# Performance work log

Measured on AMD Instinct MI355X. Metric: run time of the kernel, lower is better.

The kernel has to match this reference:

```python
import jax, jax.numpy as jnp
import numpy as np

B, S, d, D = 128, 1024, 64, 64  # batch, seq_len, physical dim, bond dim


def setup_inputs() -> dict:
    key = jax.random.key(0)
    k1, k2, k3, k4 = jax.random.split(key, 4)
    k_core = (d * D * D) ** (-0.5)
    k_vec = d ** (-0.5)
    core = k_core * jax.random.normal(k1, (d, D, D), dtype=jnp.float32)
    left_boundary = k_vec * jax.random.normal(k2, (D,), dtype=jnp.float32)
    right_boundary = k_vec * jax.random.normal(k3, (D,), dtype=jnp.float32)
    X = jax.random.randint(k4, (B, S), 0, d, dtype=jnp.int32)
    return {"X": X, "core": core, "left_boundary": left_boundary,
            "right_boundary": right_boundary}


def reference(X, core, left_boundary, right_boundary):
    """Faithful JAX version of TTrain._log_contract_at_batch (homogeneous).

    X: [B, S] int category indices; core: [d, D, D]; boundaries: [D].
    Returns logprobs: [B].
    The per-step normalization (infinity-norm) + accumulated log-norm trick of
    the original is preserved exactly; the final
    log((exp(lognorm) * out)**2) is computed in the mathematically identical
    stable form 2*(lognorm + log|out|).
    """
    batch = X.shape[0]
    lb = jnp.broadcast_to(left_boundary, (batch, left_boundary.shape[0]))  # [B, D]
    Z0 = jnp.max(jnp.abs(lb), axis=1)                                      # [B]
    c0 = lb / Z0[:, None]
    logn0 = jnp.log(Z0)

    def step(carry, x_t):
        c, logn = carry                       # c: [B, D]
        w_t = core[x_t]                       # gather selected cores: [B, D, D]
        ct = jnp.einsum('bi,bij->bj', c, w_t)  # [B, D]
        Zt = jnp.max(jnp.abs(ct), axis=1)      # [B] infinity norm
        return (ct / Zt[:, None], logn + jnp.log(Zt)), None

    (c, logn), _ = jax.lax.scan(step, (c0, logn0), X.T)  # scan over seq axis
    out = jnp.einsum('bi,i->b', c, right_boundary)        # [B]
    logprobs = 2.0 * (logn + jnp.log(jnp.abs(out)))
    return logprobs
```

## Files before the change

### kernel.cpp

```cpp
#include <hip/hip_runtime.h>
#include <math.h>


#define TT_S 1024
#define TT_D 64
#define NCHUNK 32
#define CLEN 32

typedef __attribute__((ext_vector_type(8))) short short8;
typedef __attribute__((ext_vector_type(4))) float float4v;
typedef __attribute__((ext_vector_type(4))) unsigned uint4v;
typedef __attribute__((ext_vector_type(2))) unsigned uint2v;

static __device__ __forceinline__ short8 as_short8(uint4v u) {
    union { uint4v u; short8 s; } x; x.u = u; return x.s;
}

__global__ __launch_bounds__(64) void tt_prep(
    const float* __restrict__ core, short* __restrict__ tblA,
    short* __restrict__ tblBt)
{
    const int x = blockIdx.x, l = threadIdx.x;
    const int n = l & 15, q = l >> 4;
    const float* W = core + x * 4096;

    #pragma unroll
    for (int I = 0; I < 4; ++I)
        #pragma unroll
        for (int Kp = 0; Kp < 2; ++Kp) {
            short8 v;
            const int row = 16 * I + n;
            const int c0 = 32 * Kp + 4 * q;
            #pragma unroll
            for (int j = 0; j < 8; ++j) {
                const int col = c0 + 16 * (j >> 2) + (j & 3);
                v[j] = (short)(__float_as_uint(W[row * 64 + col]) >> 16);
            }
            *(short8*)(tblA + ((size_t)(x * 8 + I * 2 + Kp) * 64 + l) * 8) = v;
        }
    #pragma unroll
    for (int Kp = 0; Kp < 2; ++Kp)
        #pragma unroll
        for (int J = 0; J < 4; ++J) {
            short8 v;
            const int col = 16 * J + n;
            const int r0 = 32 * Kp + 4 * q;
            #pragma unroll
            for (int j = 0; j < 8; ++j) {
                const int row = r0 + 16 * (j >> 2) + (j & 3);
                v[j] = (short)(__float_as_uint(W[row * 64 + col]) >> 16);
            }
            *(short8*)(tblBt + ((size_t)(x * 8 + Kp * 4 + J) * 64 + l) * 8) = v;
        }
}

__global__ __launch_bounds__(64, 4) void tt_stage1(
    const int* __restrict__ X, const short* __restrict__ tblA,
    const short* __restrict__ tblBt, short* __restrict__ PT,
    float* __restrict__ ln1)
{
    const int w = blockIdx.x;
    const int b = w / NCHUNK, chunk = w % NCHUNK;
    const int l = threadIdx.x, n = l & 15, q = l >> 4;
    const int* Xc = X + b * TT_S + chunk * CLEN;

    const float4v zero = {0.f, 0.f, 0.f, 0.f};
    float4v acc[4][4];
    short8 Bf[8], Af[8];
    float logn = 0.f;

    #define LOAD_FRAGS(DST, TBL, XIDX)                                        \
    {   const short8* p_ = (const short8*)((TBL) + (size_t)(XIDX) * 4096) + l; \
        _Pragma("unroll")                                                     \
        for (int f_ = 0; f_ < 8; ++f_) (DST)[f_] = p_[f_ * 64]; }

    #define MFMA_ALL(ABUF)                                                    \
        _Pragma("unroll")                                                     \
        for (int I_ = 0; I_ < 4; ++I_)                                        \
            _Pragma("unroll")                                                 \
            for (int J_ = 0; J_ < 4; ++J_) {                                  \
                float4v c0_ = __builtin_amdgcn_mfma_f32_16x16x32_bf16(        \
                    (ABUF)[2 * I_ + 0], Bf[J_], zero, 0, 0, 0);               \
                acc[I_][J_] = __builtin_amdgcn_mfma_f32_16x16x32_bf16(        \
                    (ABUF)[2 * I_ + 1], Bf[4 + J_], c0_, 0, 0, 0);            \
            }

    #define PACK_BF()                                                         \
        _Pragma("unroll")                                                     \
        for (int Kp_ = 0; Kp_ < 2; ++Kp_)                                     \
            _Pragma("unroll")                                                 \
            for (int J_ = 0; J_ < 4; ++J_) {                                  \
                uint4v u_;                                                    \
                u_[0] = __builtin_amdgcn_perm(                                \
                    __float_as_uint(acc[2 * Kp_][J_][1]),                     \
                    __float_as_uint(acc[2 * Kp_][J_][0]), 0x07060302u);       \
                u_[1] = __builtin_amdgcn_perm(                                \
                    __float_as_uint(acc[2 * Kp_][J_][3]),                     \
                    __float_as_uint(acc[2 * Kp_][J_][2]), 0x07060302u);       \
                u_[2] = __builtin_amdgcn_perm(                                \
                    __float_as_uint(acc[2 * Kp_ + 1][J_][1]),                 \
                    __float_as_uint(acc[2 * Kp_ + 1][J_][0]), 0x07060302u);   \
                u_[3] = __builtin_amdgcn_perm(                                \
                    __float_as_uint(acc[2 * Kp_ + 1][J_][3]),                 \
                    __float_as_uint(acc[2 * Kp_ + 1][J_][2]), 0x07060302u);   \
                Bf[Kp_ * 4 + J_] = as_short8(u_);                             \
            }

    #define RENORM()                                                          \
    {   float Z_ = 0.f;                                                       \
        _Pragma("unroll")                                                     \
        for (int I_ = 0; I_ < 4; ++I_)                                        \
            _Pragma("unroll")                                                 \
            for (int J_ = 0; J_ < 4; ++J_)                                    \
                _Pragma("unroll")                                             \
                for (int r_ = 0; r_ < 4; ++r_)                                \
                    Z_ = fmaxf(Z_, fabsf(acc[I_][J_][r_]));                   \
        _Pragma("unroll")                                                     \
        for (int m_ = 32; m_; m_ >>= 1) Z_ = fmaxf(Z_, __shfl_xor(Z_, m_));   \
        logn += logf(Z_);                                                     \
        const float rZ_ = 1.0f / Z_;                                          \
        _Pragma("unroll")                                                     \
        for (int I_ = 0; I_ < 4; ++I_)                                        \
            _Pragma("unroll")                                                 \
            for (int J_ = 0; J_ < 4; ++J_)                                    \
                _Pragma("unroll")                                             \
                for (int r_ = 0; r_ < 4; ++r_) acc[I_][J_][r_] *= rZ_; }

    LOAD_FRAGS(Bf, tblBt, Xc[CLEN - 1])
    LOAD_FRAGS(Af, tblA, Xc[CLEN - 2])
    MFMA_ALL(Af)

    #pragma unroll 1
    for (int s = 1; s < CLEN - 1; ++s) {
        LOAD_FRAGS(Af, tblA, Xc[CLEN - 2 - s])
        asm volatile("" ::: "memory");
        if ((s & 7) == 0) RENORM()
        PACK_BF()
        MFMA_ALL(Af)
    }

    {
        float Z = 0.f;
        #pragma unroll
        for (int I = 0; I < 4; ++I)
            #pragma unroll
            for (int J = 0; J < 4; ++J)
                #pragma unroll
                for (int r = 0; r < 4; ++r) Z = fmaxf(Z, fabsf(acc[I][J][r]));
        #pragma unroll
        for (int m = 32; m; m >>= 1) Z = fmaxf(Z, __shfl_xor(Z, m));
        logn += logf(Z);
        const float rZ = 1.0f / Z;
        short* base = PT + (size_t)w * 4096;
        #pragma unroll
        for (int I = 0; I < 4; ++I)
            #pragma unroll
            for (int J = 0; J < 4; ++J) {
                float4v v = acc[I][J];
                #pragma unroll
                for (int r = 0; r < 4; ++r) v[r] *= rZ;
                uint2v dd;
                dd[0] = __builtin_amdgcn_perm(__float_as_uint(v[1]),
                                              __float_as_uint(v[0]), 0x07060302u);
                dd[1] = __builtin_amdgcn_perm(__float_as_uint(v[3]),
                                              __float_as_uint(v[2]), 0x07060302u);
                *(uint2v*)(base + (16 * J + n) * 64 + 16 * I + 4 * q) = dd;
            }
        if (l == 0) ln1[w] = logn;
    }
    #undef LOAD_FRAGS
    #undef MFMA_ALL
    #undef PACK_BF
    #undef RENORM
}

__global__ __launch_bounds__(64, 1) void tt_stage2(
    const short* __restrict__ PT, const float* __restrict__ ln1,
    const float* __restrict__ lb, const float* __restrict__ rb,
    float* __restrict__ out)
{
    __shared__ float cb[64];
    const int b = blockIdx.x, j = threadIdx.x;

    float c = lb[j];
    float Z = fabsf(c);
    #pragma unroll
    for (int m = 32; m; m >>= 1) Z = fmaxf(Z, __shfl_xor(Z, m));
    float logn = logf(Z);
    c *= (1.0f / Z);

    float ln = (j < NCHUNK) ? ln1[b * NCHUNK + j] : 0.f;
    #pragma unroll
    for (int m = 32; m; m >>= 1) ln += __shfl_xor(ln, m);
    logn += ln;

    const short* base = PT + (size_t)b * NCHUNK * 4096 + j * 64;

    short8 bufA[8], bufB[8];
    #pragma unroll
    for (int f = 0; f < 8; ++f) bufA[f] = ((const short8*)base)[f];

    #define S2_STEP(BUF)                                                      \
    {                                                                         \
        cb[j] = c;                                                            \
        asm volatile("s_waitcnt lgkmcnt(0)" ::: "memory");                    \
        float a0 = 0.f, a1 = 0.f, a2 = 0.f, a3 = 0.f;                         \
        _Pragma("unroll")                                                     \
        for (int f = 0; f < 8; ++f) {                                         \
            union { short8 s; uint4v u; } uu; uu.s = (BUF)[f];                \
            const float4v cv0 = *(const float4v*)(cb + 8 * f);                \
            const float4v cv1 = *(const float4v*)(cb + 8 * f + 4);            \
            a0 = fmaf(cv0[0], __uint_as_float(uu.u[0] << 16), a0);            \
            a1 = fmaf(cv0[1], __uint_as_float(uu.u[0] & 0xffff0000u), a1);    \
            a2 = fmaf(cv0[2], __uint_as_float(uu.u[1] << 16), a2);            \
            a3 = fmaf(cv0[3], __uint_as_float(uu.u[1] & 0xffff0000u), a3);    \
            a0 = fmaf(cv1[0], __uint_as_float(uu.u[2] << 16), a0);            \
            a1 = fmaf(cv1[1], __uint_as_float(uu.u[2] & 0xffff0000u), a1);    \
            a2 = fmaf(cv1[2], __uint_as_float(uu.u[3] << 16), a2);            \
            a3 = fmaf(cv1[3], __uint_as_float(uu.u[3] & 0xffff0000u), a3);    \
        }                                                                     \
        float cn = (a0 + a1) + (a2 + a3);                                     \
        float Zl = fabsf(cn);                                                 \
        _Pragma("unroll")                                                     \
        for (int m = 32; m; m >>= 1) Zl = fmaxf(Zl, __shfl_xor(Zl, m));       \
        logn += logf(Zl);                                                     \
        c = cn * (1.0f / Zl);                                                 \
    }

    #pragma unroll 1
    for (int k = 0; k < NCHUNK; k += 2) {
        {   const short8* p = (const short8*)(base + (size_t)(k + 1) * 4096);
            #pragma unroll
            for (int f = 0; f < 8; ++f) bufB[f] = p[f];
        }
        asm volatile("" ::: "memory");
        S2_STEP(bufA)
        {   const int kn = (k + 2 < NCHUNK) ? (k + 2) : (NCHUNK - 1);
            const short8* p = (const short8*)(base + (size_t)kn * 4096);
            #pragma unroll
            for (int f = 0; f < 8; ++f) bufA[f] = p[f];
        }
        asm volatile("" ::: "memory");
        S2_STEP(bufB)
    }
    #undef S2_STEP

    float dot = c * rb[j];
    #pragma unroll
    for (int m = 32; m; m >>= 1) dot += __shfl_xor(dot, m);
    if (j == 0) out[b] = 2.0f * (logn + logf(fabsf(dot)));
}

__global__ __launch_bounds__(256) void tt_transpose(
    const float* __restrict__ core, float* __restrict__ coreT)
{
    __shared__ float tile[64][65];
    const int x = blockIdx.x;
    const float* src = core + x * 4096;
    float* dst = coreT + x * 4096;
    const int r0 = threadIdx.x >> 6, cc = threadIdx.x & 63;
    #pragma unroll
    for (int k = 0; k < 16; ++k) tile[r0 + 4 * k][cc] = src[(r0 + 4 * k) * 64 + cc];
    __syncthreads();
    #pragma unroll
    for (int k = 0; k < 16; ++k) dst[(r0 + 4 * k) * 64 + cc] = tile[cc][r0 + 4 * k];
}

__global__ __launch_bounds__(64, 1) void ttrain_chain2(
    const int* __restrict__ X, const float* __restrict__ coreT,
    const float* __restrict__ lb, const float* __restrict__ rb,
    float* __restrict__ out)
{
    __shared__ float cbuf[2][64];
    const int b = blockIdx.x, j = threadIdx.x;
    const int* Xrow = X + b * TT_S;
    float c = lb[j];
    float Z = fabsf(c);
    #pragma unroll
    for (int m = 32; m; m >>= 1) Z = fmaxf(Z, __shfl_xor(Z, m));
    float logn = logf(Z);
    c *= (1.0f / Z);
    const float* colbase = coreT + j * 64;
    int xs_cur = Xrow[j];
    int xs_nxt = Xrow[64 + j];
    float4 wA[16], wB[16];
    {
        const int x0 = Xrow[0];
        const float4* p = (const float4*)(colbase + x0 * 4096);
        #pragma unroll
        for (int k = 0; k < 16; ++k) wA[k] = p[k];
    }
    #define TT_STEP(WCUR, WNXT, SLOT, XNEXT, T)                              \
    {                                                                        \
        cbuf[SLOT][j] = c;                                                   \
        {                                                                    \
            const float4* pre = (const float4*)(colbase + (XNEXT) * 4096);   \
            _Pragma("unroll")                                                \
            for (int k = 0; k < 16; ++k) WNXT[k] = pre[k];                   \
        }                                                                    \
        asm volatile("s_waitcnt lgkmcnt(0)" ::: "memory");                   \
        float a0 = 0.f, a1 = 0.f, a2 = 0.f, a3 = 0.f;                        \
        const float4* cb2 = (const float4*)cbuf[SLOT];                       \
        _Pragma("unroll")                                                    \
        for (int k = 0; k < 16; ++k) {                                       \
            float4 cv = cb2[k];                                              \
            a0 = fmaf(cv.x, WCUR[k].x, a0);                                  \
            a1 = fmaf(cv.y, WCUR[k].y, a1);                                  \
            a2 = fmaf(cv.z, WCUR[k].z, a2);                                  \
            a3 = fmaf(cv.w, WCUR[k].w, a3);                                  \
        }                                                                    \
        float cn = (a0 + a1) + (a2 + a3);                                    \
        if (((T) & 7) == 7) {                                                \
            float Zl = fabsf(cn);                                            \
            _Pragma("unroll")                                                \
            for (int m = 32; m; m >>= 1) Zl = fmaxf(Zl, __shfl_xor(Zl, m));  \
            logn += logf(Zl);                                                \
            cn *= (1.0f / Zl);                                               \
        }                                                                    \
        c = cn;                                                              \
    }
    for (int tc = 0; tc < TT_S; tc += 64) {
        #pragma unroll 1
        for (int u = 0; u < 64; u += 2) {
            const int x1 = __builtin_amdgcn_readlane(xs_cur, u + 1);
            TT_STEP(wA, wB, 0, x1, tc + u)
            const int src2 = (u + 2 < 64) ? xs_cur : xs_nxt;
            const int x2 = __builtin_amdgcn_readlane(src2, (u + 2) & 63);
            TT_STEP(wB, wA, 1, x2, tc + u + 1)
        }
        xs_cur = xs_nxt;
        const int nc = tc + 128;
        xs_nxt = Xrow[((nc < TT_S) ? nc : 0) + j];
    }
    #undef TT_STEP
    float dot = c * rb[j];
    #pragma unroll
    for (int m = 32; m; m >>= 1) dot += __shfl_xor(dot, m);
    if (j == 0) out[b] = 2.0f * (logn + logf(fabsf(dot)));
}

extern "C" void kernel_launch(void* const* d_in, const int* in_sizes, int n_in,
                              void* d_out, int out_size, void* d_ws, size_t ws_size,
                              hipStream_t stream) {
    const int*   X    = (const int*)d_in[0];
    const float* core = (const float*)d_in[1];
    const float* lb   = (const float*)d_in[2];
    const float* rb   = (const float*)d_in[3];
    float* out = (float*)d_out;

    const int B = in_sizes[0] / TT_S;
    const size_t tblBytes = (size_t)64 * 8 * 64 * 8 * sizeof(short);
    const size_t ptBytes  = (size_t)B * NCHUNK * 4096 * sizeof(short);
    const size_t lnBytes  = (size_t)B * NCHUNK * sizeof(float);
    const size_t need = 2 * tblBytes + ptBytes + lnBytes;

    if (ws_size >= need) {
        char* w = (char*)d_ws;
        short* tblA  = (short*)w;
        short* tblBt = (short*)(w + tblBytes);
        short* PT    = (short*)(w + 2 * tblBytes);
        float* ln1   = (float*)(w + 2 * tblBytes + ptBytes);
        tt_prep<<<64, 64, 0, stream>>>(core, tblA, tblBt);
        tt_stage1<<<B * NCHUNK, 64, 0, stream>>>(X, tblA, tblBt, PT, ln1);
        tt_stage2<<<B, 64, 0, stream>>>(PT, ln1, lb, rb, out);
    } else if (ws_size >= (size_t)64 * 4096 * sizeof(float)) {
        float* coreT = (float*)d_ws;
        tt_transpose<<<64, 256, 0, stream>>>(core, coreT);
        ttrain_chain2<<<B, TT_D, 0, stream>>>(X, coreT, lb, rb, out);
    }
}
```

Before: 154.0 us.

## Fuse stage2 into stage1 via last-block atomic counter and double-buffer A fragments

Removes the separate stage2 launch. Each stage1 block increments a per-batch atomic counter, and the last chunk block of each batch runs the sequential combine of the chunk matrices. The stage1 inner loop also double-buffers the A fragments, so the next step's loads are issued before the current MFMAs and load latency overlaps with compute. The cost is more registers (launch bounds lowered from 4 to 3 waves), counter zeroing in the prep kernel, and a serial tail on the last block per batch.

After: 449.9 us. +192.1%, slower.

```diff
diff --git a/kernel.cpp b/kernel.cpp
--- a/kernel.cpp
+++ b/kernel.cpp
@@ -18,12 +18,17 @@
 
 __global__ __launch_bounds__(64) void tt_prep(
     const float* __restrict__ core, short* __restrict__ tblA,
-    short* __restrict__ tblBt)
+    short* __restrict__ tblBt, int* __restrict__ ctr)
 {
     const int x = blockIdx.x, l = threadIdx.x;
     const int n = l & 15, q = l >> 4;
     const float* W = core + x * 4096;
 
+    if (x == 0) {
+        #pragma unroll
+        for (int k = 0; k < 4; ++k) ctr[l + 64 * k] = 0;
+    }
+
     #pragma unroll
     for (int I = 0; I < 4; ++I)
         #pragma unroll
@@ -54,11 +59,14 @@
         }
 }
 
-__global__ __launch_bounds__(64, 4) void tt_stage1(
+__global__ __launch_bounds__(64, 3) void tt_stage1(
     const int* __restrict__ X, const short* __restrict__ tblA,
     const short* __restrict__ tblBt, short* __restrict__ PT,
-    float* __restrict__ ln1)
+    float* __restrict__ ln1, int* __restrict__ ctr,
+    const float* __restrict__ lb, const float* __restrict__ rb,
+    float* __restrict__ out)
 {
+    __shared__ float cb[64];
     const int w = blockIdx.x;
     const int b = w / NCHUNK, chunk = w % NCHUNK;
     const int l = threadIdx.x, n = l & 15, q = l >> 4;
@@ -66,7 +74,7 @@
 
     const float4v zero = {0.f, 0.f, 0.f, 0.f};
     float4v acc[4][4];
-    short8 Bf[8], Af[8];
+    short8 Bf[8], A0[8], A1[8];
     float logn = 0.f;
 
     #define LOAD_FRAGS(DST, TBL, XIDX)                                        \
@@ -127,16 +135,27 @@
                 for (int r_ = 0; r_ < 4; ++r_) acc[I_][J_][r_] *= rZ_; }
 
     LOAD_FRAGS(Bf, tblBt, Xc[CLEN - 1])
-    LOAD_FRAGS(Af, tblA, Xc[CLEN - 2])
-    MFMA_ALL(Af)
+    LOAD_FRAGS(A0, tblA, Xc[CLEN - 2])
+    LOAD_FRAGS(A1, tblA, Xc[CLEN - 3])
+
+    MFMA_ALL(A0)
+    LOAD_FRAGS(A0, tblA, Xc[CLEN - 4])
 
     #pragma unroll 1
-    for (int s = 1; s < CLEN - 1; ++s) {
-        LOAD_FRAGS(Af, tblA, Xc[CLEN - 2 - s])
-        asm volatile("" ::: "memory");
-        if ((s & 7) == 0) RENORM()
+    for (int it = 0; it < (CLEN - 2) / 2; ++it) {
         PACK_BF()
-        MFMA_ALL(Af)
+        MFMA_ALL(A1)
+        {
+            const int tn = CLEN - 6 - 2 * it;
+            LOAD_FRAGS(A1, tblA, Xc[tn < 0 ? 0 : tn])
+        }
+        if (((2 * it + 2) & 7) == 0) RENORM()
+        PACK_BF()
+        MFMA_ALL(A0)
+        {
+            const int tn = CLEN - 7 - 2 * it;
+            LOAD_FRAGS(A0, tblA, Xc[tn < 0 ? 0 : tn])
+        }
     }
 
     {
@@ -172,37 +191,36 @@
     #undef MFMA_ALL
     #undef PACK_BF
     #undef RENORM
-}
-
-__global__ __launch_bounds__(64, 1) void tt_stage2(
-    const short* __restrict__ PT, const float* __restrict__ ln1,
-    const float* __restrict__ lb, const float* __restrict__ rb,
-    float* __restrict__ out)
-{
-    __shared__ float cb[64];
-    const int b = blockIdx.x, j = threadIdx.x;
-
-    float c = lb[j];
+
+    __threadfence();
+    int last = 0;
+    if (l == 0) last = (atomicAdd(&ctr[b], 1) == NCHUNK - 1) ? 1 : 0;
+    last = __shfl(last, 0);
+    if (!last) return;
+    __threadfence();
+
+    float c = lb[l];
     float Z = fabsf(c);
     #pragma unroll
     for (int m = 32; m; m >>= 1) Z = fmaxf(Z, __shfl_xor(Z, m));
-    float logn = logf(Z);
+    float lg = logf(Z);
     c *= (1.0f / Z);
 
-    float ln = (j < NCHUNK) ? ln1[b * NCHUNK + j] : 0.f;
-    #pragma unroll
-    for (int m = 32; m; m >>= 1) ln += __shfl_xor(ln, m);
-    logn += ln;
-
-    const short* base = PT + (size_t)b * NCHUNK * 4096 + j * 64;
-
+    {
+        float ln = (l < NCHUNK) ? ln1[b * NCHUNK + l] : 0.f;
+        #pragma unroll
+        for (int m = 32; m; m >>= 1) ln += __shfl_xor(ln, m);
+        lg += ln;
+    }
+
+    const short* base2 = PT + (size_t)b * NCHUNK * 4096 + l * 64;
     short8 bufA[8], bufB[8];
     #pragma unroll
-    for (int f = 0; f < 8; ++f) bufA[f] = ((const short8*)base)[f];
+    for (int f = 0; f < 8; ++f) bufA[f] = ((const short8*)base2)[f];
 
     #define S2_STEP(BUF)                                                      \
     {                                                                         \
-        cb[j] = c;                                                            \
+        cb[l] = c;                                                            \
         asm volatile("s_waitcnt lgkmcnt(0)" ::: "memory");                    \
         float a0 = 0.f, a1 = 0.f, a2 = 0.f, a3 = 0.f;                         \
         _Pragma("unroll")                                                     \
@@ -223,20 +241,20 @@
         float Zl = fabsf(cn);                                                 \
         _Pragma("unroll")                                                     \
         for (int m = 32; m; m >>= 1) Zl = fmaxf(Zl, __shfl_xor(Zl, m));       \
-        logn += logf(Zl);                                                     \
+        lg += logf(Zl);                                                       \
         c = cn * (1.0f / Zl);                                                 \
     }
 
     #pragma unroll 1
     for (int k = 0; k < NCHUNK; k += 2) {
-        {   const short8* p = (const short8*)(base + (size_t)(k + 1) * 4096);
+        {   const short8* p = (const short8*)(base2 + (size_t)(k + 1) * 4096);
             #pragma unroll
             for (int f = 0; f < 8; ++f) bufB[f] = p[f];
         }
         asm volatile("" ::: "memory");
         S2_STEP(bufA)
         {   const int kn = (k + 2 < NCHUNK) ? (k + 2) : (NCHUNK - 1);
-            const short8* p = (const short8*)(base + (size_t)kn * 4096);
+            const short8* p = (const short8*)(base2 + (size_t)kn * 4096);
             #pragma unroll
             for (int f = 0; f < 8; ++f) bufA[f] = p[f];
         }
@@ -245,10 +263,10 @@
     }
     #undef S2_STEP
 
-    float dot = c * rb[j];
+    float dot = c * rb[l];
     #pragma unroll
     for (int m = 32; m; m >>= 1) dot += __shfl_xor(dot, m);
-    if (j == 0) out[b] = 2.0f * (logn + logf(fabsf(dot)));
+    if (l == 0) out[b] = 2.0f * (lg + logf(fabsf(dot)));
 }
 
 __global__ __launch_bounds__(256) void tt_transpose(
@@ -352,7 +370,8 @@
     const size_t tblBytes = (size_t)64 * 8 * 64 * 8 * sizeof(short);
     const size_t ptBytes  = (size_t)B * NCHUNK * 4096 * sizeof(short);
     const size_t lnBytes  = (size_t)B * NCHUNK * sizeof(float);
-    const size_t need = 2 * tblBytes + ptBytes + lnBytes;
+    const size_t ctrBytes = 256 * sizeof(int);
+    const size_t need = 2 * tblBytes + ptBytes + lnBytes + ctrBytes;
 
     if (ws_size >= need) {
         char* w = (char*)d_ws;
@@ -360,9 +379,10 @@
         short* tblBt = (short*)(w + tblBytes);
         short* PT    = (short*)(w + 2 * tblBytes);
         float* ln1   = (float*)(w + 2 * tblBytes + ptBytes);
-        tt_prep<<<64, 64, 0, stream>>>(core, tblA, tblBt);
-        tt_stage1<<<B * NCHUNK, 64, 0, stream>>>(X, tblA, tblBt, PT, ln1);
-        tt_stage2<<<B, 64, 0, stream>>>(PT, ln1, lb, rb, out);
+        int*   ctr   = (int*)(w + 2 * tblBytes + ptBytes + lnBytes);
+        tt_prep<<<64, 64, 0, stream>>>(core, tblA, tblBt, ctr);
+        tt_stage1<<<B * NCHUNK, 64, 0, stream>>>(X, tblA, tblBt, PT, ln1, ctr,
+                                                 lb, rb, out);
     } else if (ws_size >= (size_t)64 * 4096 * sizeof(float)) {
         float* coreT = (float*)d_ws;
         tt_transpose<<<64, 256, 0, stream>>>(core, coreT);
```

## Halve chunk count, double-buffer A fragments, interleave pack with MFMA per column

Applied to the files above, without the earlier changes.

Stage1 now splits the sequence into 16 chunks of 64 steps instead of 32 of 32. It double-buffers the gathered core fragments so each load is issued two steps ahead, and it interleaves the bf16 packing of each output column with its MFMAs to shorten the dependency chain. The prep kernel now uses four waves per block instead of one. The aim is fewer stage-1 products and less stage-2 work plus better latency hiding, at the cost of half as many stage-1 waves, a longer serial chain per wave and more registers.

Result: faster. 133.5 us (-13.3%).

```diff
diff --git a/kernel.cpp b/kernel.cpp
--- a/kernel.cpp
+++ b/kernel.cpp
@@ -4,8 +4,8 @@
 
 #define TT_S 1024
 #define TT_D 64
-#define NCHUNK 32
-#define CLEN 32
+#define NCHUNK 16
+#define CLEN 64
 
 typedef __attribute__((ext_vector_type(8))) short short8;
 typedef __attribute__((ext_vector_type(4))) float float4v;
@@ -16,30 +16,34 @@
     union { uint4v u; short8 s; } x; x.u = u; return x.s;
 }
 
-__global__ __launch_bounds__(64) void tt_prep(
+__global__ __launch_bounds__(256) void tt_prep(
     const float* __restrict__ core, short* __restrict__ tblA,
     short* __restrict__ tblBt)
 {
-    const int x = blockIdx.x, l = threadIdx.x;
+    const int x = blockIdx.x;
+    const int l = threadIdx.x & 63, r = threadIdx.x >> 6;
     const int n = l & 15, q = l >> 4;
     const float* W = core + x * 4096;
 
-    #pragma unroll
-    for (int I = 0; I < 4; ++I)
-        #pragma unroll
-        for (int Kp = 0; Kp < 2; ++Kp) {
-            short8 v;
-            const int row = 16 * I + n;
-            const int c0 = 32 * Kp + 4 * q;
-            #pragma unroll
-            for (int j = 0; j < 8; ++j) {
-                const int col = c0 + 16 * (j >> 2) + (j & 3);
-                v[j] = (short)(__float_as_uint(W[row * 64 + col]) >> 16);
+    if (r < 2) {
+        #pragma unroll
+        for (int Ii = 0; Ii < 2; ++Ii) {
+            const int I = 2 * r + Ii;
+            #pragma unroll
+            for (int Kp = 0; Kp < 2; ++Kp) {
+                short8 v;
+                const int row = 16 * I + n;
+                const int c0 = 32 * Kp + 4 * q;
+                #pragma unroll
+                for (int j = 0; j < 8; ++j) {
+                    const int col = c0 + 16 * (j >> 2) + (j & 3);
+                    v[j] = (short)(__float_as_uint(W[row * 64 + col]) >> 16);
+                }
+                *(short8*)(tblA + ((size_t)(x * 8 + I * 2 + Kp) * 64 + l) * 8) = v;
             }
-            *(short8*)(tblA + ((size_t)(x * 8 + I * 2 + Kp) * 64 + l) * 8) = v;
-        }
-    #pragma unroll
-    for (int Kp = 0; Kp < 2; ++Kp)
+        }
+    } else {
+        const int Kp = r - 2;
         #pragma unroll
         for (int J = 0; J < 4; ++J) {
             short8 v;
@@ -52,22 +56,26 @@
             }
             *(short8*)(tblBt + ((size_t)(x * 8 + Kp * 4 + J) * 64 + l) * 8) = v;
         }
-}
-
-__global__ __launch_bounds__(64, 4) void tt_stage1(
+    }
+}
+
+__global__ __launch_bounds__(64, 2) void tt_stage1(
     const int* __restrict__ X, const short* __restrict__ tblA,
     const short* __restrict__ tblBt, short* __restrict__ PT,
     float* __restrict__ ln1)
 {
     const int w = blockIdx.x;
-    const int b = w / NCHUNK, chunk = w % NCHUNK;
+    const int b = w >> 4, chunk = w & 15;
     const int l = threadIdx.x, n = l & 15, q = l >> 4;
     const int* Xc = X + b * TT_S + chunk * CLEN;
 
     const float4v zero = {0.f, 0.f, 0.f, 0.f};
     float4v acc[4][4];
-    short8 Bf[8], Af[8];
+    short8 Bf[8], A0[8], A1[8];
     float logn = 0.f;
+
+    #define PK(hi, lo) __builtin_amdgcn_perm(__float_as_uint(hi),             \
+                                             __float_as_uint(lo), 0x07060302u)
 
     #define LOAD_FRAGS(DST, TBL, XIDX)                                        \
     {   const short8* p_ = (const short8*)((TBL) + (size_t)(XIDX) * 4096) + l; \
@@ -85,26 +93,28 @@
                     (ABUF)[2 * I_ + 1], Bf[4 + J_], c0_, 0, 0, 0);            \
             }
 
-    #define PACK_BF()                                                         \
-        _Pragma("unroll")                                                     \
-        for (int Kp_ = 0; Kp_ < 2; ++Kp_)                                     \
+    #define PROD(ABUF)                                                        \
+        _Pragma("unroll")                                                     \
+        for (int J_ = 0; J_ < 4; ++J_) {                                      \
+            uint4v u0_, u1_;                                                  \
+            u0_[0] = PK(acc[0][J_][1], acc[0][J_][0]);                        \
+            u0_[1] = PK(acc[0][J_][3], acc[0][J_][2]);                        \
+            u0_[2] = PK(acc[1][J_][1], acc[1][J_][0]);                        \
+            u0_[3] = PK(acc[1][J_][3], acc[1][J_][2]);                        \
+            u1_[0] = PK(acc[2][J_][1], acc[2][J_][0]);                        \
+            u1_[1] = PK(acc[2][J_][3], acc[2][J_][2]);                        \
+            u1_[2] = PK(acc[3][J_][1], acc[3][J_][0]);                        \
+            u1_[3] = PK(acc[3][J_][3], acc[3][J_][2]);                        \
+            Bf[J_] = as_short8(u0_);                                          \
+            Bf[4 + J_] = as_short8(u1_);                                      \
             _Pragma("unroll")                                                 \
-            for (int J_ = 0; J_ < 4; ++J_) {                                  \
-                uint4v u_;                                                    \
-                u_[0] = __builtin_amdgcn_perm(                                \
-                    __float_as_uint(acc[2 * Kp_][J_][1]),                     \
-                    __float_as_uint(acc[2 * Kp_][J_][0]), 0x07060302u);       \
-                u_[1] = __builtin_amdgcn_perm(                                \
-                    __float_as_uint(acc[2 * Kp_][J_][3]),                     \
-                    __float_as_uint(acc[2 * Kp_][J_][2]), 0x07060302u);       \
-                u_[2] = __builtin_amdgcn_perm(                                \
-                    __float_as_uint(acc[2 * Kp_ + 1][J_][1]),                 \
-                    __float_as_uint(acc[2 * Kp_ + 1][J_][0]), 0x07060302u);   \
-                u_[3] = __builtin_amdgcn_perm(                                \
-                    __float_as_uint(acc[2 * Kp_ + 1][J_][3]),                 \
-                    __float_as_uint(acc[2 * Kp_ + 1][J_][2]), 0x07060302u);   \
-                Bf[Kp_ * 4 + J_] = as_short8(u_);                             \
-            }
+            for (int I_ = 0; I_ < 4; ++I_) {                                  \
+                float4v c0_ = __builtin_amdgcn_mfma_f32_16x16x32_bf16(        \
+                    (ABUF)[2 * I_ + 0], Bf[J_], zero, 0, 0, 0);               \
+                acc[I_][J_] = __builtin_amdgcn_mfma_f32_16x16x32_bf16(        \
+                    (ABUF)[2 * I_ + 1], Bf[4 + J_], c0_, 0, 0, 0);            \
+            }                                                                 \
+        }
 
     #define RENORM()                                                          \
     {   float Z_ = 0.f;                                                       \
@@ -127,16 +137,25 @@
                 for (int r_ = 0; r_ < 4; ++r_) acc[I_][J_][r_] *= rZ_; }
 
     LOAD_FRAGS(Bf, tblBt, Xc[CLEN - 1])
-    LOAD_FRAGS(Af, tblA, Xc[CLEN - 2])
-    MFMA_ALL(Af)
+    LOAD_FRAGS(A0, tblA, Xc[CLEN - 2])
+    LOAD_FRAGS(A1, tblA, Xc[CLEN - 3])
+
+    MFMA_ALL(A0)
+    LOAD_FRAGS(A0, tblA, Xc[CLEN - 4])
 
     #pragma unroll 1
-    for (int s = 1; s < CLEN - 1; ++s) {
-        LOAD_FRAGS(Af, tblA, Xc[CLEN - 2 - s])
-        asm volatile("" ::: "memory");
-        if ((s & 7) == 0) RENORM()
-        PACK_BF()
-        MFMA_ALL(Af)
+    for (int it = 0; it < 31; ++it) {
+        PROD(A1)
+        {
+            const int tn = 59 - 2 * it;
+            LOAD_FRAGS(A1, tblA, Xc[tn < 0 ? 0 : tn])
+        }
+        if (((2 * it + 2) & 7) == 0) RENORM()
+        PROD(A0)
+        {
+            const int tn = 58 - 2 * it;
+            LOAD_FRAGS(A0, tblA, Xc[tn < 0 ? 0 : tn])
+        }
     }
 
     {
@@ -160,18 +179,17 @@
                 #pragma unroll
                 for (int r = 0; r < 4; ++r) v[r] *= rZ;
                 uint2v dd;
-                dd[0] = __builtin_amdgcn_perm(__float_as_uint(v[1]),
-                                              __float_as_uint(v[0]), 0x07060302u);
-                dd[1] = __builtin_amdgcn_perm(__float_as_uint(v[3]),
-                                              __float_as_uint(v[2]), 0x07060302u);
+                dd[0] = PK(v[1], v[0]);
+                dd[1] = PK(v[3], v[2]);
                 *(uint2v*)(base + (16 * J + n) * 64 + 16 * I + 4 * q) = dd;
             }
         if (l == 0) ln1[w] = logn;
     }
     #undef LOAD_FRAGS
     #undef MFMA_ALL
-    #undef PACK_BF
+    #undef PROD
     #undef RENORM
+    #undef PK
 }
 
 __global__ __launch_bounds__(64, 1) void tt_stage2(
@@ -360,7 +378,7 @@
         short* tblBt = (short*)(w + tblBytes);
         short* PT    = (short*)(w + 2 * tblBytes);
         float* ln1   = (float*)(w + 2 * tblBytes + ptBytes);
-        tt_prep<<<64, 64, 0, stream>>>(core, tblA, tblBt);
+        tt_prep<<<64, 256, 0, stream>>>(core, tblA, tblBt);
         tt_stage1<<<B * NCHUNK, 64, 0, stream>>>(X, tblA, tblBt, PT, ln1);
         tt_stage2<<<B, 64, 0, stream>>>(PT, ln1, lb, rb, out);
     } else if (ws_size >= (size_t)64 * 4096 * sizeof(float)) {
```
